# Optimization experiments

Hardware: AMD Instinct MI355X
Metric: run time of the kernel (lower is better)

The kernel has to match this reference:

```python
import jax, jax.numpy as jnp
import numpy as np

DEPTH, HEADS, DIM, DHEAD, MLP = 4, 16, 1024, 64, 4096
B, N, M = 4, 1024, 1024
EPS = 1e-5


def layer_norm(x, w, b):
    mu = jnp.mean(x, axis=-1, keepdims=True)
    var = jnp.var(x, axis=-1, keepdims=True)
    return (x - mu) * jax.lax.rsqrt(var + EPS) * w + b


def setup_inputs() -> dict:
    key = jax.random.key(0)
    ks = jax.random.split(key, 16)
    inner = HEADS * DHEAD
    s = lambda fan_in: 1.0 / np.sqrt(fan_in)
    # weights stored in (in, out) layout: y = x @ W + b
    return {
        "x": jax.random.normal(ks[0], (B, N, DIM), jnp.float32),
        "m": jax.random.normal(ks[1], (B, M, DIM), jnp.float32),
        "Wq": jax.random.normal(ks[2], (DEPTH, DIM, inner), jnp.float32) * s(DIM),
        "Wk": jax.random.normal(ks[3], (DEPTH, DIM, inner), jnp.float32) * s(DIM),
        "Wv": jax.random.normal(ks[4], (DEPTH, DIM, inner), jnp.float32) * s(DIM),
        "Wo": jax.random.normal(ks[5], (DEPTH, inner, DIM), jnp.float32) * s(inner),
        "bo": jnp.zeros((DEPTH, DIM), jnp.float32),
        "ln1_w": jnp.ones((DEPTH, DIM), jnp.float32),
        "ln1_b": jnp.zeros((DEPTH, DIM), jnp.float32),
        "W1": jax.random.normal(ks[6], (DEPTH, DIM, MLP), jnp.float32) * s(DIM),
        "b1": jnp.zeros((DEPTH, MLP), jnp.float32),
        "W2": jax.random.normal(ks[7], (DEPTH, MLP, DIM), jnp.float32) * s(MLP),
        "b2": jnp.zeros((DEPTH, DIM), jnp.float32),
        "ln2_w": jnp.ones((DEPTH, DIM), jnp.float32),
        "ln2_b": jnp.zeros((DEPTH, DIM), jnp.float32),
    }


def reference(x, m, Wq, Wk, Wv, Wo, bo, ln1_w, ln1_b, W1, b1, W2, b2, ln2_w, ln2_b):
    scale = DIM ** (-0.5)  # NOTE: original scales by dim**-0.5, not dim_head**-0.5
    for i in range(DEPTH):
        # cross-attention block (PreNorm on x only; m is used raw, as in source)
        h = layer_norm(x, ln1_w[i], ln1_b[i])
        q = jnp.einsum('bnd,de->bne', h, Wq[i]).reshape(B, N, HEADS, DHEAD)
        k = jnp.einsum('bmd,de->bme', m, Wk[i]).reshape(B, M, HEADS, DHEAD)
        v = jnp.einsum('bmd,de->bme', m, Wv[i]).reshape(B, M, HEADS, DHEAD)
        dots = jnp.einsum('bihd,bjhd->bhij', q, k) * scale
        attn = jax.nn.softmax(dots, axis=-1)
        out = jnp.einsum('bhij,bjhd->bihd', attn, v).reshape(B, N, HEADS * DHEAD)
        x = x + jnp.einsum('bne,ed->bnd', out, Wo[i]) + bo[i]
        # feed-forward block
        h2 = layer_norm(x, ln2_w[i], ln2_b[i])
        ff = jax.nn.gelu(jnp.einsum('bnd,df->bnf', h2, W1[i]) + b1[i], approximate=False)
        x = x + jnp.einsum('bnf,fd->bnd', ff, W2[i]) + b2[i]
    return x
```

## Files before the change

### kernel.cpp

```cpp
#include <hip/hip_runtime.h>
#include <hip/hip_bf16.h>
#include <math.h>

typedef __hip_bfloat16 bf16;
typedef __attribute__((ext_vector_type(8))) short bf16x8;
typedef __attribute__((ext_vector_type(4))) float f32x4;

#define DEPTH  4
#define HEADS  16
#define DIM    1024
#define DHEAD  64
#define MLPD   4096
#define BB     4
#define NN     1024
#define MMK    1024
#define ROWS   (BB*NN)

__device__ inline float bitsbf(short s) {
  union { float f; unsigned u; } c; c.u = ((unsigned)(unsigned short)s) << 16; return c.f;
}
__device__ inline short bfbits(float f) {
  bf16 h = __float2bfloat16(f); return *(short*)&h;
}

__global__ __launch_bounds__(256) void f2b_kernel(const float* __restrict__ in, bf16* __restrict__ out, int n) {
  int i = blockIdx.x * 256 + threadIdx.x;
  if (i < n) out[i] = __float2bfloat16(in[i]);
}

__global__ __launch_bounds__(256) void transpose_f2b(const float* __restrict__ in, bf16* __restrict__ out,
                                                     int inStride, int rowOff, int colOff, int outStride) {
  __shared__ float tile[32][33];
  int n0 = blockIdx.x * 32, k0 = blockIdx.y * 32;
  int tx = threadIdx.x, ty = threadIdx.y;
  #pragma unroll
  for (int i = 0; i < 32; i += 8)
    tile[ty + i][tx] = in[(size_t)(rowOff + k0 + ty + i) * inStride + colOff + n0 + tx];
  __syncthreads();
  #pragma unroll
  for (int i = 0; i < 32; i += 8)
    out[(size_t)(n0 + ty + i) * outStride + k0 + tx] = __float2bfloat16(tile[tx][ty + i]);
}

__global__ __launch_bounds__(256) void ln_kernel(const float* __restrict__ x, const float* __restrict__ w,
                                                 const float* __restrict__ b, bf16* __restrict__ out) {
  int row = blockIdx.x, t = threadIdx.x;
  const float* xr = x + (size_t)row * DIM;
  float4 xv = *(const float4*)(xr + t * 4);
  float s  = xv.x + xv.y + xv.z + xv.w;
  float s2 = xv.x * xv.x + xv.y * xv.y + xv.z * xv.z + xv.w * xv.w;
  #pragma unroll
  for (int off = 32; off; off >>= 1) { s += __shfl_xor(s, off, 64); s2 += __shfl_xor(s2, off, 64); }
  __shared__ float sh_s[4], sh_s2[4], sh_mu, sh_rstd;
  int wid = t >> 6;
  if ((t & 63) == 0) { sh_s[wid] = s; sh_s2[wid] = s2; }
  __syncthreads();
  if (t == 0) {
    float S1 = sh_s[0] + sh_s[1] + sh_s[2] + sh_s[3];
    float S2 = sh_s2[0] + sh_s2[1] + sh_s2[2] + sh_s2[3];
    float mu = S1 * (1.0f / DIM);
    float var = S2 * (1.0f / DIM) - mu * mu;
    sh_mu = mu; sh_rstd = rsqrtf(var + 1e-5f);
  }
  __syncthreads();
  float mu = sh_mu, rstd = sh_rstd;
  float4 wv = *(const float4*)(w + t * 4);
  float4 bv = *(const float4*)(b + t * 4);
  bf16* orow = out + (size_t)row * DIM + t * 4;
  orow[0] = __float2bfloat16((xv.x - mu) * rstd * wv.x + bv.x);
  orow[1] = __float2bfloat16((xv.y - mu) * rstd * wv.y + bv.y);
  orow[2] = __float2bfloat16((xv.z - mu) * rstd * wv.z + bv.z);
  orow[3] = __float2bfloat16((xv.w - mu) * rstd * wv.w + bv.w);
}

#define MODE_PLAIN 0
#define MODE_GELU  1
#define MODE_RES   2
#define LDK 40

__global__ __launch_bounds__(256) void gemm_kernel(const bf16* __restrict__ A, const bf16* __restrict__ Bt,
                                                   const float* __restrict__ bias, bf16* __restrict__ outb,
                                                   float* __restrict__ resf, int N, int K, int mode) {
  __shared__ bf16 As[64][LDK];
  __shared__ bf16 Bs[64][LDK];
  int t = threadIdx.x;
  int col0 = blockIdx.x * 64, row0 = blockIdx.y * 64;
  int lane = t & 63, wid = t >> 6;
  int wm = (wid >> 1) * 32, wn = (wid & 1) * 32;
  int l15 = lane & 15, quad = lane >> 4;
  int am = t >> 2, ak = (t & 3) * 8;

  f32x4 acc00 = {}, acc01 = {}, acc10 = {}, acc11 = {};

  const bf16* aptr = A  + (size_t)(row0 + am) * K + ak;
  const bf16* bptr = Bt + (size_t)(col0 + am) * K + ak;

  for (int k0 = 0; k0 < K; k0 += 32) {
    *(bf16x8*)(&As[am][ak]) = *(const bf16x8*)(aptr + k0);
    *(bf16x8*)(&Bs[am][ak]) = *(const bf16x8*)(bptr + k0);
    __syncthreads();
    bf16x8 a0 = *(const bf16x8*)(&As[wm + l15][quad * 8]);
    bf16x8 a1 = *(const bf16x8*)(&As[wm + 16 + l15][quad * 8]);
    bf16x8 b0 = *(const bf16x8*)(&Bs[wn + l15][quad * 8]);
    bf16x8 b1 = *(const bf16x8*)(&Bs[wn + 16 + l15][quad * 8]);
    acc00 = __builtin_amdgcn_mfma_f32_16x16x32_bf16(a0, b0, acc00, 0, 0, 0);
    acc01 = __builtin_amdgcn_mfma_f32_16x16x32_bf16(a0, b1, acc01, 0, 0, 0);
    acc10 = __builtin_amdgcn_mfma_f32_16x16x32_bf16(a1, b0, acc10, 0, 0, 0);
    acc11 = __builtin_amdgcn_mfma_f32_16x16x32_bf16(a1, b1, acc11, 0, 0, 0);
    __syncthreads();
  }

  f32x4 accs[2][2] = {{acc00, acc01}, {acc10, acc11}};
  #pragma unroll
  for (int i = 0; i < 2; ++i) {
    #pragma unroll
    for (int j = 0; j < 2; ++j) {
      int gcol = col0 + wn + j * 16 + l15;
      float bval = (mode != MODE_PLAIN && bias != nullptr) ? bias[gcol] : 0.0f;
      #pragma unroll
      for (int r = 0; r < 4; ++r) {
        int grow = row0 + wm + i * 16 + quad * 4 + r;
        float val = accs[i][j][r];
        size_t idx = (size_t)grow * N + gcol;
        if (mode == MODE_RES) {
          resf[idx] = resf[idx] + val + bval;
        } else {
          if (mode == MODE_GELU) {
            float u = val + bval;
            val = 0.5f * u * (1.0f + erff(u * 0.70710678118654752f));
          }
          outb[idx] = __float2bfloat16(val);
        }
      }
    }
  }
}

#define ALDP 72

__global__ __launch_bounds__(256) void attn_mfma_kernel(const bf16* __restrict__ q, const bf16* __restrict__ k,
                                                        const bf16* __restrict__ v, bf16* __restrict__ o) {
  __shared__ __align__(16) short Kl[64][ALDP];
  __shared__ __align__(16) short Vt[64][ALDP];
  __shared__ __align__(16) short Pl[64][ALDP];

  int t = threadIdx.x;
  int lane = t & 63, w = t >> 6;
  int l15 = lane & 15, quad = lane >> 4;
  int qt = blockIdx.x;
  int bh = blockIdx.y;
  int b = bh >> 4, hh = bh & 15;

  bf16x8 qfrag[2];
  {
    const bf16* qp = q + (size_t)(b * NN + qt * 64 + w * 16 + l15) * DIM + hh * DHEAD + quad * 8;
    #pragma unroll
    for (int ks = 0; ks < 2; ++ks) {
      bf16x8 raw = *(const bf16x8*)(qp + ks * 32);
      bf16x8 sc;
      #pragma unroll
      for (int e = 0; e < 8; ++e) sc[e] = bfbits(bitsbf(raw[e]) * 0.03125f);
      qfrag[ks] = sc;
    }
  }

  f32x4 Oacc[4] = {{}, {}, {}, {}};
  float mrow[4] = {-1e30f, -1e30f, -1e30f, -1e30f};
  float lrow[4] = {0.f, 0.f, 0.f, 0.f};

  int srow = t >> 2, sc0 = (t & 3) * 16;

  for (int kt = 0; kt < MMK / 64; ++kt) {
    __syncthreads();
    {
      const bf16* kp = k + (size_t)(b * MMK + kt * 64 + srow) * DIM + hh * DHEAD + sc0;
      *(bf16x8*)&Kl[srow][sc0]     = *(const bf16x8*)kp;
      *(bf16x8*)&Kl[srow][sc0 + 8] = *(const bf16x8*)(kp + 8);
      const bf16* vp = v + (size_t)(b * MMK + kt * 64 + srow) * DIM + hh * DHEAD + sc0;
      bf16x8 v0 = *(const bf16x8*)vp;
      bf16x8 v1 = *(const bf16x8*)(vp + 8);
      #pragma unroll
      for (int e = 0; e < 8; ++e) {
        Vt[sc0 + e][srow]     = v0[e];
        Vt[sc0 + 8 + e][srow] = v1[e];
      }
    }
    __syncthreads();

    f32x4 S[4] = {{}, {}, {}, {}};
    #pragma unroll
    for (int ks = 0; ks < 2; ++ks) {
      #pragma unroll
      for (int j = 0; j < 4; ++j) {
        bf16x8 bfr = *(const bf16x8*)&Kl[j * 16 + l15][ks * 32 + quad * 8];
        S[j] = __builtin_amdgcn_mfma_f32_16x16x32_bf16(qfrag[ks], bfr, S[j], 0, 0, 0);
      }
    }

    #pragma unroll
    for (int r = 0; r < 4; ++r) {
      float tm = fmaxf(fmaxf(S[0][r], S[1][r]), fmaxf(S[2][r], S[3][r]));
      tm = fmaxf(tm, __shfl_xor(tm, 1, 64));
      tm = fmaxf(tm, __shfl_xor(tm, 2, 64));
      tm = fmaxf(tm, __shfl_xor(tm, 4, 64));
      tm = fmaxf(tm, __shfl_xor(tm, 8, 64));
      float mn = fmaxf(mrow[r], tm);
      float alpha = __expf(mrow[r] - mn);
      mrow[r] = mn;
      float rs = 0.f;
      #pragma unroll
      for (int j = 0; j < 4; ++j) {
        float p = __expf(S[j][r] - mn);
        S[j][r] = p;
        rs += p;
      }
      rs += __shfl_xor(rs, 1, 64);
      rs += __shfl_xor(rs, 2, 64);
      rs += __shfl_xor(rs, 4, 64);
      rs += __shfl_xor(rs, 8, 64);
      lrow[r] = lrow[r] * alpha + rs;
      #pragma unroll
      for (int j = 0; j < 4; ++j) {
        Oacc[j][r] *= alpha;
        Pl[w * 16 + quad * 4 + r][j * 16 + l15] = bfbits(S[j][r]);
      }
    }
    __syncthreads();

    #pragma unroll
    for (int ks = 0; ks < 2; ++ks) {
      bf16x8 pa = *(const bf16x8*)&Pl[w * 16 + l15][ks * 32 + quad * 8];
      #pragma unroll
      for (int j = 0; j < 4; ++j) {
        bf16x8 vb = *(const bf16x8*)&Vt[j * 16 + l15][ks * 32 + quad * 8];
        Oacc[j] = __builtin_amdgcn_mfma_f32_16x16x32_bf16(pa, vb, Oacc[j], 0, 0, 0);
      }
    }
  }

  #pragma unroll
  for (int r = 0; r < 4; ++r) {
    float inv = 1.0f / lrow[r];
    bf16* op = o + (size_t)(b * NN + qt * 64 + w * 16 + quad * 4 + r) * DIM + hh * DHEAD;
    #pragma unroll
    for (int j = 0; j < 4; ++j)
      op[j * 16 + l15] = __float2bfloat16(Oacc[j][r] * inv);
  }
}

extern "C" void kernel_launch(void* const* d_in, const int* in_sizes, int n_in,
                              void* d_out, int out_size, void* d_ws, size_t ws_size,
                              hipStream_t stream) {
  const float* x_in = (const float*)d_in[0];
  const float* m    = (const float*)d_in[1];
  const float* Wq   = (const float*)d_in[2];
  const float* Wk   = (const float*)d_in[3];
  const float* Wv   = (const float*)d_in[4];
  const float* Wo   = (const float*)d_in[5];
  const float* bo   = (const float*)d_in[6];
  const float* ln1w = (const float*)d_in[7];
  const float* ln1b = (const float*)d_in[8];
  const float* W1   = (const float*)d_in[9];
  const float* b1   = (const float*)d_in[10];
  const float* W2   = (const float*)d_in[11];
  const float* b2   = (const float*)d_in[12];
  const float* ln2w = (const float*)d_in[13];
  const float* ln2b = (const float*)d_in[14];

  float* xf = (float*)d_out;

  char* ws = (char*)d_ws;
  bf16* h   = (bf16*)(ws + 0);
  bf16* mb  = (bf16*)(ws + (8u  << 20));
  bf16* qb  = (bf16*)(ws + (16u << 20));
  bf16* kb  = (bf16*)(ws + (24u << 20));
  bf16* vb  = (bf16*)(ws + (32u << 20));
  bf16* ffh = (bf16*)(ws + (16u << 20));
  bf16* wt  = (bf16*)(ws + (40u << 20));

  const int NTOK = ROWS * DIM;

  hipMemcpyAsync(xf, x_in, (size_t)NTOK * sizeof(float), hipMemcpyDeviceToDevice, stream);
  f2b_kernel<<<dim3((NTOK + 255) / 256), dim3(256), 0, stream>>>(m, mb, NTOK);

  dim3 blk(256);
  dim3 tblk(32, 8);
  dim3 gemm_n1(DIM / 64, ROWS / 64);
  dim3 gemm_n2(2048 / 64, ROWS / 64);
  dim3 tr_1k(DIM / 32, DIM / 32);
  dim3 tr_w1(2048 / 32, DIM / 32);
  dim3 tr_w2(DIM / 32, 2048 / 32);
  dim3 attn_grid(NN / 64, BB * HEADS);

  for (int L = 0; L < DEPTH; ++L) {
    const float* WqL = Wq + (size_t)L * DIM * DIM;
    const float* WkL = Wk + (size_t)L * DIM * DIM;
    const float* WvL = Wv + (size_t)L * DIM * DIM;
    const float* WoL = Wo + (size_t)L * DIM * DIM;
    const float* W1L = W1 + (size_t)L * DIM * MLPD;
    const float* W2L = W2 + (size_t)L * MLPD * DIM;

    ln_kernel<<<dim3(ROWS), blk, 0, stream>>>(xf, ln1w + L * DIM, ln1b + L * DIM, h);

    transpose_f2b<<<tr_1k, tblk, 0, stream>>>(WqL, wt, DIM, 0, 0, DIM);
    gemm_kernel<<<gemm_n1, blk, 0, stream>>>(h, wt, nullptr, qb, nullptr, DIM, DIM, MODE_PLAIN);
    transpose_f2b<<<tr_1k, tblk, 0, stream>>>(WkL, wt, DIM, 0, 0, DIM);
    gemm_kernel<<<gemm_n1, blk, 0, stream>>>(mb, wt, nullptr, kb, nullptr, DIM, DIM, MODE_PLAIN);
    transpose_f2b<<<tr_1k, tblk, 0, stream>>>(WvL, wt, DIM, 0, 0, DIM);
    gemm_kernel<<<gemm_n1, blk, 0, stream>>>(mb, wt, nullptr, vb, nullptr, DIM, DIM, MODE_PLAIN);

    attn_mfma_kernel<<<attn_grid, blk, 0, stream>>>(qb, kb, vb, h);

    transpose_f2b<<<tr_1k, tblk, 0, stream>>>(WoL, wt, DIM, 0, 0, DIM);
    gemm_kernel<<<gemm_n1, blk, 0, stream>>>(h, wt, bo + L * DIM, nullptr, xf, DIM, DIM, MODE_RES);

    ln_kernel<<<dim3(ROWS), blk, 0, stream>>>(xf, ln2w + L * DIM, ln2b + L * DIM, h);

    for (int half = 0; half < 2; ++half) {
      transpose_f2b<<<tr_w1, tblk, 0, stream>>>(W1L, wt, MLPD, 0, half * 2048, DIM);
      gemm_kernel<<<gemm_n2, blk, 0, stream>>>(h, wt, b1 + (size_t)L * MLPD + half * 2048, ffh, nullptr,
                                               2048, DIM, MODE_GELU);
      transpose_f2b<<<tr_w2, tblk, 0, stream>>>(W2L, wt, DIM, half * 2048, 0, 2048);
      gemm_kernel<<<gemm_n1, blk, 0, stream>>>(ffh, wt, (half == 0) ? (b2 + (size_t)L * DIM) : nullptr,
                                               nullptr, xf, DIM, 2048, MODE_RES);
    }
  }
}
```

Before: 1.819 ms.

## Enlarge GEMM tiles to 128x128 and load tiles via direct global-to-LDS

Replaces the 64x64 MFMA GEMM with a 128x128 tile kernel where each wave computes a 64x64 sub-tile using a 4x4 grid of 16x16x32 MFMAs. Tiles are staged with global_load_lds, which writes global memory straight into LDS without going through registers. The larger tile raises arithmetic intensity and cuts the global traffic per FLOP. In exchange the LDS layout is unpadded, so fragment reads may hit bank conflicts. There is also fewer blocks (256 for the N=1024 GEMMs), no double buffering, and higher register use.

```diff
diff --git a/kernel.cpp b/kernel.cpp
--- a/kernel.cpp
+++ b/kernel.cpp
@@ -21,6 +21,11 @@
 }
 __device__ inline short bfbits(float f) {
   bf16 h = __float2bfloat16(f); return *(short*)&h;
+}
+
+__device__ inline void gload_lds16(const bf16* g, bf16* l) {
+  __builtin_amdgcn_global_load_lds((const __attribute__((address_space(1))) unsigned int*)g,
+                                   (__attribute__((address_space(3))) unsigned int*)l, 16, 0, 0);
 }
 
 __global__ __launch_bounds__(256) void f2b_kernel(const float* __restrict__ in, bf16* __restrict__ out, int n) {
@@ -76,51 +81,63 @@
 #define MODE_PLAIN 0
 #define MODE_GELU  1
 #define MODE_RES   2
-#define LDK 40
-
-__global__ __launch_bounds__(256) void gemm_kernel(const bf16* __restrict__ A, const bf16* __restrict__ Bt,
-                                                   const float* __restrict__ bias, bf16* __restrict__ outb,
-                                                   float* __restrict__ resf, int N, int K, int mode) {
-  __shared__ bf16 As[64][LDK];
-  __shared__ bf16 Bs[64][LDK];
+#define BM 128
+#define BN 128
+#define BK 32
+
+__global__ __launch_bounds__(256) void gemm128_kernel(const bf16* __restrict__ A, const bf16* __restrict__ Bt,
+                                                      const float* __restrict__ bias, bf16* __restrict__ outb,
+                                                      float* __restrict__ resf, int N, int K, int mode) {
+  __shared__ __align__(16) bf16 As[BM * BK];
+  __shared__ __align__(16) bf16 Bs[BN * BK];
   int t = threadIdx.x;
-  int col0 = blockIdx.x * 64, row0 = blockIdx.y * 64;
-  int lane = t & 63, wid = t >> 6;
-  int wm = (wid >> 1) * 32, wn = (wid & 1) * 32;
-  int l15 = lane & 15, quad = lane >> 4;
-  int am = t >> 2, ak = (t & 3) * 8;
-
-  f32x4 acc00 = {}, acc01 = {}, acc10 = {}, acc11 = {};
-
-  const bf16* aptr = A  + (size_t)(row0 + am) * K + ak;
-  const bf16* bptr = Bt + (size_t)(col0 + am) * K + ak;
-
-  for (int k0 = 0; k0 < K; k0 += 32) {
-    *(bf16x8*)(&As[am][ak]) = *(const bf16x8*)(aptr + k0);
-    *(bf16x8*)(&Bs[am][ak]) = *(const bf16x8*)(bptr + k0);
-    __syncthreads();
-    bf16x8 a0 = *(const bf16x8*)(&As[wm + l15][quad * 8]);
-    bf16x8 a1 = *(const bf16x8*)(&As[wm + 16 + l15][quad * 8]);
-    bf16x8 b0 = *(const bf16x8*)(&Bs[wn + l15][quad * 8]);
-    bf16x8 b1 = *(const bf16x8*)(&Bs[wn + 16 + l15][quad * 8]);
-    acc00 = __builtin_amdgcn_mfma_f32_16x16x32_bf16(a0, b0, acc00, 0, 0, 0);
-    acc01 = __builtin_amdgcn_mfma_f32_16x16x32_bf16(a0, b1, acc01, 0, 0, 0);
-    acc10 = __builtin_amdgcn_mfma_f32_16x16x32_bf16(a1, b0, acc10, 0, 0, 0);
-    acc11 = __builtin_amdgcn_mfma_f32_16x16x32_bf16(a1, b1, acc11, 0, 0, 0);
-    __syncthreads();
-  }
-
-  f32x4 accs[2][2] = {{acc00, acc01}, {acc10, acc11}};
-  #pragma unroll
-  for (int i = 0; i < 2; ++i) {
-    #pragma unroll
-    for (int j = 0; j < 2; ++j) {
+  int w = t >> 6, l = t & 63;
+  int l15 = l & 15, quad = l >> 4;
+  int col0 = blockIdx.x * BN, row0 = blockIdx.y * BM;
+  int wm = (w >> 1) * 64, wn = (w & 1) * 64;
+
+  f32x4 acc[4][4] = {};
+
+  int sm = w * 16 + (l >> 2);
+  int sk = (l & 3) * 8;
+  const bf16* ag0 = A  + (size_t)(row0 + sm) * K + sk;
+  const bf16* ag1 = A  + (size_t)(row0 + 64 + sm) * K + sk;
+  const bf16* bg0 = Bt + (size_t)(col0 + sm) * K + sk;
+  const bf16* bg1 = Bt + (size_t)(col0 + 64 + sm) * K + sk;
+  bf16* lA0 = As + w * 512;
+  bf16* lA1 = As + 2048 + w * 512;
+  bf16* lB0 = Bs + w * 512;
+  bf16* lB1 = Bs + 2048 + w * 512;
+
+  for (int k0 = 0; k0 < K; k0 += BK) {
+    gload_lds16(ag0 + k0, lA0);
+    gload_lds16(ag1 + k0, lA1);
+    gload_lds16(bg0 + k0, lB0);
+    gload_lds16(bg1 + k0, lB1);
+    __syncthreads();
+    bf16x8 af[4], bfr[4];
+    #pragma unroll
+    for (int i = 0; i < 4; ++i) af[i]  = *(const bf16x8*)&As[(wm + i * 16 + l15) * BK + quad * 8];
+    #pragma unroll
+    for (int j = 0; j < 4; ++j) bfr[j] = *(const bf16x8*)&Bs[(wn + j * 16 + l15) * BK + quad * 8];
+    #pragma unroll
+    for (int i = 0; i < 4; ++i)
+      #pragma unroll
+      for (int j = 0; j < 4; ++j)
+        acc[i][j] = __builtin_amdgcn_mfma_f32_16x16x32_bf16(af[i], bfr[j], acc[i][j], 0, 0, 0);
+    __syncthreads();
+  }
+
+  #pragma unroll
+  for (int i = 0; i < 4; ++i) {
+    #pragma unroll
+    for (int j = 0; j < 4; ++j) {
       int gcol = col0 + wn + j * 16 + l15;
       float bval = (mode != MODE_PLAIN && bias != nullptr) ? bias[gcol] : 0.0f;
       #pragma unroll
       for (int r = 0; r < 4; ++r) {
         int grow = row0 + wm + i * 16 + quad * 4 + r;
-        float val = accs[i][j][r];
+        float val = acc[i][j][r];
         size_t idx = (size_t)grow * N + gcol;
         if (mode == MODE_RES) {
           resf[idx] = resf[idx] + val + bval;
@@ -285,8 +302,8 @@
 
   dim3 blk(256);
   dim3 tblk(32, 8);
-  dim3 gemm_n1(DIM / 64, ROWS / 64);
-  dim3 gemm_n2(2048 / 64, ROWS / 64);
+  dim3 gemm_n1(DIM / BN, ROWS / BM);
+  dim3 gemm_n2(2048 / BN, ROWS / BM);
   dim3 tr_1k(DIM / 32, DIM / 32);
   dim3 tr_w1(2048 / 32, DIM / 32);
   dim3 tr_w2(DIM / 32, 2048 / 32);
@@ -303,26 +320,26 @@
     ln_kernel<<<dim3(ROWS), blk, 0, stream>>>(xf, ln1w + L * DIM, ln1b + L * DIM, h);
 
     transpose_f2b<<<tr_1k, tblk, 0, stream>>>(WqL, wt, DIM, 0, 0, DIM);
-    gemm_kernel<<<gemm_n1, blk, 0, stream>>>(h, wt, nullptr, qb, nullptr, DIM, DIM, MODE_PLAIN);
+    gemm128_kernel<<<gemm_n1, blk, 0, stream>>>(h, wt, nullptr, qb, nullptr, DIM, DIM, MODE_PLAIN);
     transpose_f2b<<<tr_1k, tblk, 0, stream>>>(WkL, wt, DIM, 0, 0, DIM);
-    gemm_kernel<<<gemm_n1, blk, 0, stream>>>(mb, wt, nullptr, kb, nullptr, DIM, DIM, MODE_PLAIN);
+    gemm128_kernel<<<gemm_n1, blk, 0, stream>>>(mb, wt, nullptr, kb, nullptr, DIM, DIM, MODE_PLAIN);
     transpose_f2b<<<tr_1k, tblk, 0, stream>>>(WvL, wt, DIM, 0, 0, DIM);
-    gemm_kernel<<<gemm_n1, blk, 0, stream>>>(mb, wt, nullptr, vb, nullptr, DIM, DIM, MODE_PLAIN);
+    gemm128_kernel<<<gemm_n1, blk, 0, stream>>>(mb, wt, nullptr, vb, nullptr, DIM, DIM, MODE_PLAIN);
 
     attn_mfma_kernel<<<attn_grid, blk, 0, stream>>>(qb, kb, vb, h);
 
     transpose_f2b<<<tr_1k, tblk, 0, stream>>>(WoL, wt, DIM, 0, 0, DIM);
-    gemm_kernel<<<gemm_n1, blk, 0, stream>>>(h, wt, bo + L * DIM, nullptr, xf, DIM, DIM, MODE_RES);
+    gemm128_kernel<<<gemm_n1, blk, 0, stream>>>(h, wt, bo + L * DIM, nullptr, xf, DIM, DIM, MODE_RES);
 
     ln_kernel<<<dim3(ROWS), blk, 0, stream>>>(xf, ln2w + L * DIM, ln2b + L * DIM, h);
 
     for (int half = 0; half < 2; ++half) {
       transpose_f2b<<<tr_w1, tblk, 0, stream>>>(W1L, wt, MLPD, 0, half * 2048, DIM);
-      gemm_kernel<<<gemm_n2, blk, 0, stream>>>(h, wt, b1 + (size_t)L * MLPD + half * 2048, ffh, nullptr,
-                                               2048, DIM, MODE_GELU);
+      gemm128_kernel<<<gemm_n2, blk, 0, stream>>>(h, wt, b1 + (size_t)L * MLPD + half * 2048, ffh, nullptr,
+                                                  2048, DIM, MODE_GELU);
       transpose_f2b<<<tr_w2, tblk, 0, stream>>>(W2L, wt, DIM, half * 2048, 0, 2048);
-      gemm_kernel<<<gemm_n1, blk, 0, stream>>>(ffh, wt, (half == 0) ? (b2 + (size_t)L * DIM) : nullptr,
-                                               nullptr, xf, DIM, 2048, MODE_RES);
-    }
-  }
-}
+      gemm128_kernel<<<gemm_n1, blk, 0, stream>>>(ffh, wt, (half == 0) ? (b2 + (size_t)L * DIM) : nullptr,
+                                                  nullptr, xf, DIM, 2048, MODE_RES);
+    }
+  }
+}
```

New measurement: 2.101 ms. 1.16x slower.
